# Optimization experiments

Hardware: AMD Instinct MI355X
Metric: run time of the kernel (lower is better)

Reference implementation:

```python
import jax, jax.numpy as jnp
import numpy as np

HIDDEN = 512
HEADS = 8
HEAD_DIM = HIDDEN // HEADS


def setup_inputs() -> dict:
    key = jax.random.key(0)
    ks = jax.random.split(key, 9)
    B, S = 4, 2048
    scale = 1.0 / np.sqrt(HIDDEN)
    x = jax.random.normal(ks[0], (B, S, HIDDEN), dtype=jnp.float32)
    Wq = jax.random.normal(ks[1], (HIDDEN, HIDDEN), dtype=jnp.float32) * scale
    Wk = jax.random.normal(ks[2], (HIDDEN, HIDDEN), dtype=jnp.float32) * scale
    Wv = jax.random.normal(ks[3], (HIDDEN, HIDDEN), dtype=jnp.float32) * scale
    Wo = jax.random.normal(ks[4], (HIDDEN, HIDDEN), dtype=jnp.float32) * scale
    bq = jax.random.normal(ks[5], (HIDDEN,), dtype=jnp.float32) * 0.01
    bk = jax.random.normal(ks[6], (HIDDEN,), dtype=jnp.float32) * 0.01
    bv = jax.random.normal(ks[7], (HIDDEN,), dtype=jnp.float32) * 0.01
    bo = jax.random.normal(ks[8], (HIDDEN,), dtype=jnp.float32) * 0.01
    return {"x": x, "Wq": Wq, "bq": bq, "Wk": Wk, "bk": bk,
            "Wv": Wv, "bv": bv, "Wo": Wo, "bo": bo}


def reference(x, Wq, bq, Wk, bk, Wv, bv, Wo, bo):
    B, S, _ = x.shape
    # project and split heads: [B, H, S, D]
    def split_heads(t):
        return t.reshape(B, S, HEADS, HEAD_DIM).transpose(0, 2, 1, 3)
    Q = split_heads(x @ Wq.T + bq)
    K = split_heads(x @ Wk.T + bk)
    V = split_heads(x @ Wv.T + bv)
    scores = jnp.einsum("bhsd,bhtd->bhst", Q, K) / jnp.sqrt(
        jnp.array(HEAD_DIM, dtype=x.dtype))
    attn = jax.nn.softmax(scores, axis=-1)  # dropout is identity in eval
    ctx = jnp.einsum("bhst,bhtd->bhsd", attn, V)
    ctx = ctx.transpose(0, 2, 1, 3).reshape(B, S, HIDDEN)
    return ctx @ Wo.T + bo
```

## Files before the change

kernel.cpp:

```cpp
#include <hip/hip_runtime.h>
#include <stdint.h>

#define HID 512
#define NH 8
#define HD 64
#define BB 4
#define SS 2048

typedef unsigned short u16;
typedef __attribute__((ext_vector_type(8))) short short8;
typedef __attribute__((ext_vector_type(4))) float f32x4;

#define MFMA16(a, b, c) __builtin_amdgcn_mfma_f32_16x16x32_bf16((a), (b), (c), 0, 0, 0)

__device__ __forceinline__ u16 f2bf(float f) {
  union { float f; uint32_t u; } v; v.f = f;
  return (u16)((v.u + 0x7fffu + ((v.u >> 16) & 1u)) >> 16);
}

__device__ __forceinline__ void gl_lds16(const u16* g, u16* l) {
  __builtin_amdgcn_global_load_lds(
      (const __attribute__((address_space(1))) unsigned int*)g,
      (__attribute__((address_space(3))) unsigned int*)l, 16, 0, 0);
}

__global__ void prep(const float* __restrict__ x,
                     const float* __restrict__ w0, const float* __restrict__ w1,
                     const float* __restrict__ w2, const float* __restrict__ w3,
                     u16* __restrict__ xb,
                     u16* __restrict__ o0, u16* __restrict__ o1,
                     u16* __restrict__ o2, u16* __restrict__ o3) {
  const int bid = blockIdx.x;
  const float* in;
  u16* out;
  int base;
  if (bid < 4096) {
    in = x; out = xb; base = bid * 1024;
  } else {
    const int z = (bid - 4096) >> 8;
    base = ((bid - 4096) & 255) * 1024;
    in = (z == 0) ? w0 : (z == 1) ? w1 : (z == 2) ? w2 : w3;
    out = (z == 0) ? o0 : (z == 1) ? o1 : (z == 2) ? o2 : o3;
  }
  const int i = base + threadIdx.x * 4;
  float4 v = *(const float4*)(in + i);
  ushort4 o;
  o.x = f2bf(v.x); o.y = f2bf(v.y); o.z = f2bf(v.z); o.w = f2bf(v.w);
  *(ushort4*)(out + i) = o;
}

__global__ __launch_bounds__(256, 3)
void qkv_gemm(const u16* __restrict__ xb,
              const u16* __restrict__ wq, const u16* __restrict__ wk, const u16* __restrict__ wv,
              const float* __restrict__ bq, const float* __restrict__ bk, const float* __restrict__ bv,
              u16* __restrict__ Q, u16* __restrict__ K, u16* __restrict__ Vt) {
  __shared__ u16 sA[2][128 * 32];
  __shared__ u16 sB[2][128 * 32];
  const int tid = threadIdx.x;
  const int lane = tid & 63;
  const int wave = tid >> 6;
  const int l15 = lane & 15;
  const int quad = lane >> 4;
  const int wm = wave >> 1, wn = wave & 1;
  const int z = blockIdx.z;

  const float* bias = (z == 0) ? bq : (z == 1) ? bk : bv;
  const float scale = (z == 0) ? 0.18033688011112042f : 1.0f;

  const u16* Arows = (z == 2) ? wv : xb;
  const u16* Brows = (z == 2) ? xb : ((z == 0) ? wq : wk);
  const int am0 = (z == 2) ? (blockIdx.y * 128) : (blockIdx.x * 128);
  const int bn0 = (z == 2) ? (blockIdx.x * 128) : (blockIdx.y * 128);

  const int srow = tid >> 2;
  const int sg = (tid & 3) ^ ((srow >> 1) & 3);
  const u16* gA = Arows + (am0 + srow) * 512 + sg * 8;
  const u16* gB = Brows + (bn0 + srow) * 512 + sg * 8;

  const int fsw = (quad ^ ((l15 >> 1) & 3)) * 8;
  int aoff[4], boff[4];
#pragma unroll
  for (int t = 0; t < 4; ++t) {
    aoff[t] = (wm * 64 + t * 16 + l15) * 32 + fsw;
    boff[t] = (wn * 64 + t * 16 + l15) * 32 + fsw;
  }

  f32x4 acc[4][4] = {};

  gl_lds16(gA, &sA[0][wave * 512]);
  gl_lds16(gA + 64 * 512, &sA[0][2048 + wave * 512]);
  gl_lds16(gB, &sB[0][wave * 512]);
  gl_lds16(gB + 64 * 512, &sB[0][2048 + wave * 512]);
  __syncthreads();

  for (int kk = 0; kk < 16; ++kk) {
    const int cur = kk & 1;
    if (kk < 15) {
      const int nxt = cur ^ 1;
      const int k0 = (kk + 1) * 32;
      gl_lds16(gA + k0, &sA[nxt][wave * 512]);
      gl_lds16(gA + k0 + 64 * 512, &sA[nxt][2048 + wave * 512]);
      gl_lds16(gB + k0, &sB[nxt][wave * 512]);
      gl_lds16(gB + k0 + 64 * 512, &sB[nxt][2048 + wave * 512]);
    }
    short8 af[4], bf[4];
#pragma unroll
    for (int t = 0; t < 4; ++t) af[t] = *(const short8*)&sA[cur][aoff[t]];
#pragma unroll
    for (int t = 0; t < 4; ++t) bf[t] = *(const short8*)&sB[cur][boff[t]];
#pragma unroll
    for (int mi = 0; mi < 4; ++mi)
#pragma unroll
      for (int ni = 0; ni < 4; ++ni)
        acc[mi][ni] = MFMA16(af[mi], bf[ni], acc[mi][ni]);
    __syncthreads();
  }

  if (z != 2) {
    u16* dst = (z == 0) ? Q : K;
#pragma unroll
    for (int mi = 0; mi < 4; ++mi) {
#pragma unroll
      for (int ni = 0; ni < 4; ++ni) {
        const int col = bn0 + wn * 64 + ni * 16 + l15;
        const float bs = bias[col];
#pragma unroll
        for (int i = 0; i < 4; ++i) {
          const int row = am0 + wm * 64 + mi * 16 + quad * 4 + i;
          const float v = (acc[mi][ni][i] + bs) * scale;
          const int b = row >> 11, s = row & 2047;
          const int h = col >> 6, d = col & 63;
          dst[(((size_t)(b * 8 + h) * 2048 + s) << 6) + d] = f2bf(v);
        }
      }
    }
  } else {
#pragma unroll
    for (int mi = 0; mi < 4; ++mi) {
#pragma unroll
      for (int i = 0; i < 4; ++i) {
        const int o = am0 + wm * 64 + mi * 16 + quad * 4 + i;
        const float bs = bias[o];
        const int h = o >> 6, d = o & 63;
#pragma unroll
        for (int ni = 0; ni < 4; ++ni) {
          const int r = bn0 + wn * 64 + ni * 16 + l15;
          const int b = r >> 11, s = r & 2047;
          Vt[(((size_t)(b * 8 + h) * 64 + d) << 11) + s] = f2bf(acc[mi][ni][i] + bs);
        }
      }
    }
  }
}

__global__ __launch_bounds__(512, 4)
void attn(const u16* __restrict__ Q, const u16* __restrict__ K,
          const u16* __restrict__ Vt, u16* __restrict__ ctx) {
  __shared__ u16 sK[2][64 * 64];
  __shared__ u16 sV[2][64 * 64];
  __shared__ u16 sP[128 * 64];
  const int tid = threadIdx.x;
  const int lane = tid & 63;
  const int wave = tid >> 6;
  const int l15 = lane & 15;
  const int quad = lane >> 4;
  const int qt = blockIdx.x;
  const int bh = blockIdx.y;

  const u16* Qb = Q + (size_t)bh * SS * HD;
  const u16* Kb = K + (size_t)bh * SS * HD;
  const u16* Vb = Vt + (size_t)bh * HD * SS;

  short8 qf[2];
  {
    const int r = qt * 128 + wave * 16 + l15;
    qf[0] = *(const short8*)(Qb + r * 64 + quad * 8);
    qf[1] = *(const short8*)(Qb + r * 64 + 32 + quad * 8);
  }

  short8 ones;
#pragma unroll
  for (int j = 0; j < 8; ++j) ones[j] = (short)0x3F80;

  f32x4 oacc[4] = {};
  f32x4 lsum = {};

  const int prow = (wave * 16 + l15) * 64;
  int xp[2];
#pragma unroll
  for (int kt = 0; kt < 2; ++kt) xp[kt] = ((kt * 4 + quad) ^ (l15 & 7)) * 8;

  const int tK = tid >> 3;
  const int dcK = (tid & 7) ^ (tK & 7);
  const u16* gK = Kb + tK * 64 + dcK * 8;
  const u16* gV = Vb + tK * 2048 + dcK * 8;

  gl_lds16(gK, &sK[0][wave * 512]);
  gl_lds16(gV, &sV[0][wave * 512]);
  __syncthreads();

  for (int tt = 0; tt < 32; ++tt) {
    const int cur = tt & 1;
    if (tt < 31) {
      const int nxt = cur ^ 1;
      gl_lds16(gK + (tt + 1) * 4096, &sK[nxt][wave * 512]);
      gl_lds16(gV + (tt + 1) * 64, &sV[nxt][wave * 512]);
    }

    f32x4 sacc[4] = {};
#pragma unroll
    for (int ni = 0; ni < 4; ++ni) {
      const short8 b0 = *(const short8*)&sK[cur][(ni * 16 + l15) * 64 + ((quad) ^ (l15 & 7)) * 8];
      const short8 b1 = *(const short8*)&sK[cur][(ni * 16 + l15) * 64 + ((4 + quad) ^ (l15 & 7)) * 8];
      sacc[ni] = MFMA16(qf[0], b0, sacc[ni]);
      sacc[ni] = MFMA16(qf[1], b1, sacc[ni]);
    }

#pragma unroll
    for (int i = 0; i < 4; ++i) {
      const int wrow = wave * 16 + quad * 4 + i;
      const int rx7 = (quad * 4 + i) & 7;
      const int base = wrow * 64 + (l15 & 7);
#pragma unroll
      for (int ni = 0; ni < 4; ++ni) {
        const float p = __builtin_amdgcn_exp2f(sacc[ni][i]);
        const uint32_t u = __builtin_bit_cast(uint32_t, p);
        sP[base + (((ni * 2 + (l15 >> 3)) ^ rx7) << 3)] = (u16)(u >> 16);
      }
    }

#pragma unroll
    for (int kt = 0; kt < 2; ++kt) {
      const short8 a = *(const short8*)&sP[prow + xp[kt]];
      lsum = MFMA16(a, ones, lsum);
#pragma unroll
      for (int nd = 0; nd < 4; ++nd) {
        const short8 bvv = *(const short8*)&sV[cur][(nd * 16 + l15) * 64 +
                                                   ((kt * 4 + quad) ^ (l15 & 7)) * 8];
        oacc[nd] = MFMA16(a, bvv, oacc[nd]);
      }
    }
    __syncthreads();
  }

  float inv[4];
#pragma unroll
  for (int i = 0; i < 4; ++i) inv[i] = __builtin_amdgcn_rcpf(lsum[i]);

  const int b = bh >> 3, h = bh & 7;
#pragma unroll
  for (int nd = 0; nd < 4; ++nd)
#pragma unroll
    for (int i = 0; i < 4; ++i) {
      const int s = qt * 128 + wave * 16 + quad * 4 + i;
      const int d = nd * 16 + l15;
      const float v = oacc[nd][i] * inv[i];
      ctx[((size_t)(b * 2048 + s) << 9) + h * 64 + d] = f2bf(v);
    }
}

__global__ __launch_bounds__(256, 2)
void out_gemm(const u16* __restrict__ A, const u16* __restrict__ W,
              const float* __restrict__ bias, float* __restrict__ out) {
  __shared__ u16 sA[2][128 * 32];
  __shared__ u16 sB[2][64 * 32];
  const int tid = threadIdx.x;
  const int lane = tid & 63;
  const int wave = tid >> 6;
  const int l15 = lane & 15;
  const int quad = lane >> 4;
  const int bm = blockIdx.x, bn = blockIdx.y;

  const int srow = tid >> 2;
  const int sg = (tid & 3) ^ ((srow >> 1) & 3);
  const u16* gA = A + (bm * 128 + srow) * 512 + sg * 8;
  const u16* gB = W + (bn * 64 + srow) * 512 + sg * 8;

  const int fsw = (quad ^ ((l15 >> 1) & 3)) * 8;
  int aoff[2], boff[4];
#pragma unroll
  for (int t = 0; t < 2; ++t) aoff[t] = (wave * 32 + t * 16 + l15) * 32 + fsw;
#pragma unroll
  for (int t = 0; t < 4; ++t) boff[t] = (t * 16 + l15) * 32 + fsw;

  f32x4 acc[2][4] = {};

  gl_lds16(gA, &sA[0][wave * 512]);
  gl_lds16(gA + 64 * 512, &sA[0][2048 + wave * 512]);
  gl_lds16(gB, &sB[0][wave * 512]);
  __syncthreads();

  for (int kk = 0; kk < 16; ++kk) {
    const int cur = kk & 1;
    if (kk < 15) {
      const int nxt = cur ^ 1;
      const int k0 = (kk + 1) * 32;
      gl_lds16(gA + k0, &sA[nxt][wave * 512]);
      gl_lds16(gA + k0 + 64 * 512, &sA[nxt][2048 + wave * 512]);
      gl_lds16(gB + k0, &sB[nxt][wave * 512]);
    }
    short8 af[2], bf[4];
#pragma unroll
    for (int t = 0; t < 2; ++t) af[t] = *(const short8*)&sA[cur][aoff[t]];
#pragma unroll
    for (int t = 0; t < 4; ++t) bf[t] = *(const short8*)&sB[cur][boff[t]];
#pragma unroll
    for (int mi = 0; mi < 2; ++mi)
#pragma unroll
      for (int ni = 0; ni < 4; ++ni)
        acc[mi][ni] = MFMA16(af[mi], bf[ni], acc[mi][ni]);
    __syncthreads();
  }

#pragma unroll
  for (int mi = 0; mi < 2; ++mi) {
#pragma unroll
    for (int ni = 0; ni < 4; ++ni) {
      const int col = bn * 64 + ni * 16 + l15;
      const float bs = bias[col];
#pragma unroll
      for (int i = 0; i < 4; ++i) {
        const int row = bm * 128 + wave * 32 + mi * 16 + quad * 4 + i;
        out[(size_t)row * 512 + col] = acc[mi][ni][i] + bs;
      }
    }
  }
}

extern "C" void kernel_launch(void* const* d_in, const int* in_sizes, int n_in,
                              void* d_out, int out_size, void* d_ws, size_t ws_size,
                              hipStream_t stream) {
  const float* x = (const float*)d_in[0];
  const float* Wq = (const float*)d_in[1];
  const float* bq = (const float*)d_in[2];
  const float* Wk = (const float*)d_in[3];
  const float* bk = (const float*)d_in[4];
  const float* Wv = (const float*)d_in[5];
  const float* bv = (const float*)d_in[6];
  const float* Wo = (const float*)d_in[7];
  const float* bo = (const float*)d_in[8];
  float* out = (float*)d_out;

  char* ws = (char*)d_ws;
  u16* xb  = (u16*)(ws);
  u16* wqb = (u16*)(ws + (8u << 20));
  u16* wkb = (u16*)(ws + (8u << 20) + (512u << 10));
  u16* wvb = (u16*)(ws + (9u << 20));
  u16* wob = (u16*)(ws + (9u << 20) + (512u << 10));
  u16* Qb  = (u16*)(ws + (10u << 20));
  u16* Kb  = (u16*)(ws + (18u << 20));
  u16* Vtb = (u16*)(ws + (26u << 20));
  u16* ctx = (u16*)(ws + (34u << 20));

  prep<<<5120, 256, 0, stream>>>(x, Wq, Wk, Wv, Wo, xb, wqb, wkb, wvb, wob);
  qkv_gemm<<<dim3(64, 4, 3), 256, 0, stream>>>(xb, wqb, wkb, wvb, bq, bk, bv, Qb, Kb, Vtb);
  attn<<<dim3(16, 32), 512, 0, stream>>>(Qb, Kb, Vtb, ctx);
  out_gemm<<<dim3(64, 8), 256, 0, stream>>>(ctx, wob, bo, out);
}
```

Before: 169.6 us.

## Deepen LDS pipelines with vmcnt waits and remap blocks to XCDs

Replaces the double-buffered LDS loads in the QKV GEMM, attention and output GEMM with triple/quad buffering. Each loop now waits on a partial vmcnt and a single barrier instead of a full __syncthreads, so more global->LDS loads stay in flight. It also flattens the grids and remaps block IDs so blocks that share data land on the same XCD, to improve L2 reuse. Costs are more LDS per block, which may lower occupancy, and correctness now depends on hand-written waitcnt encodings and barrier placement.

```diff
diff --git a/kernel.cpp b/kernel.cpp
--- a/kernel.cpp
+++ b/kernel.cpp
@@ -12,6 +12,11 @@
 typedef __attribute__((ext_vector_type(4))) float f32x4;
 
 #define MFMA16(a, b, c) __builtin_amdgcn_mfma_f32_16x16x32_bf16((a), (b), (c), 0, 0, 0)
+
+#define WAIT_VM4() __builtin_amdgcn_s_waitcnt(0xF74)
+#define WAIT_VM3() __builtin_amdgcn_s_waitcnt(0xF73)
+#define PIPE_BARRIER() do { asm volatile("" ::: "memory"); \
+  __builtin_amdgcn_s_barrier(); asm volatile("" ::: "memory"); } while (0)
 
 __device__ __forceinline__ u16 f2bf(float f) {
   union { float f; uint32_t u; } v; v.f = f;
@@ -54,23 +59,30 @@
               const u16* __restrict__ wq, const u16* __restrict__ wk, const u16* __restrict__ wv,
               const float* __restrict__ bq, const float* __restrict__ bk, const float* __restrict__ bv,
               u16* __restrict__ Q, u16* __restrict__ K, u16* __restrict__ Vt) {
-  __shared__ u16 sA[2][128 * 32];
-  __shared__ u16 sB[2][128 * 32];
+  __shared__ u16 sA[3][4096];
+  __shared__ u16 sB[3][4096];
   const int tid = threadIdx.x;
   const int lane = tid & 63;
   const int wave = tid >> 6;
   const int l15 = lane & 15;
   const int quad = lane >> 4;
   const int wm = wave >> 1, wn = wave & 1;
-  const int z = blockIdx.z;
+
+  const int L = blockIdx.x;
+  const int xcd = L & 7;
+  const int slot = L >> 3;
+  const int bm = xcd * 8 + (slot & 7);
+  const int r2 = slot >> 3;
+  const int bn = r2 & 3;
+  const int z = r2 >> 2;
 
   const float* bias = (z == 0) ? bq : (z == 1) ? bk : bv;
   const float scale = (z == 0) ? 0.18033688011112042f : 1.0f;
 
   const u16* Arows = (z == 2) ? wv : xb;
   const u16* Brows = (z == 2) ? xb : ((z == 0) ? wq : wk);
-  const int am0 = (z == 2) ? (blockIdx.y * 128) : (blockIdx.x * 128);
-  const int bn0 = (z == 2) ? (blockIdx.x * 128) : (blockIdx.y * 128);
+  const int am0 = (z == 2) ? (bn * 128) : (bm * 128);
+  const int bn0 = (z == 2) ? (bm * 128) : (bn * 128);
 
   const int srow = tid >> 2;
   const int sg = (tid & 3) ^ ((srow >> 1) & 3);
@@ -87,22 +99,28 @@
 
   f32x4 acc[4][4] = {};
 
-  gl_lds16(gA, &sA[0][wave * 512]);
-  gl_lds16(gA + 64 * 512, &sA[0][2048 + wave * 512]);
-  gl_lds16(gB, &sB[0][wave * 512]);
-  gl_lds16(gB + 64 * 512, &sB[0][2048 + wave * 512]);
-  __syncthreads();
+#pragma unroll
+  for (int t = 0; t < 2; ++t) {
+    const int k0 = t * 32;
+    gl_lds16(gA + k0, &sA[t][wave * 512]);
+    gl_lds16(gA + k0 + 64 * 512, &sA[t][2048 + wave * 512]);
+    gl_lds16(gB + k0, &sB[t][wave * 512]);
+    gl_lds16(gB + k0 + 64 * 512, &sB[t][2048 + wave * 512]);
+  }
 
   for (int kk = 0; kk < 16; ++kk) {
-    const int cur = kk & 1;
-    if (kk < 15) {
-      const int nxt = cur ^ 1;
-      const int k0 = (kk + 1) * 32;
-      gl_lds16(gA + k0, &sA[nxt][wave * 512]);
-      gl_lds16(gA + k0 + 64 * 512, &sA[nxt][2048 + wave * 512]);
-      gl_lds16(gB + k0, &sB[nxt][wave * 512]);
-      gl_lds16(gB + k0 + 64 * 512, &sB[nxt][2048 + wave * 512]);
-    }
+    WAIT_VM4();
+    PIPE_BARRIER();
+    {
+      const int tp = (kk + 2 < 16) ? kk + 2 : 15;
+      const int ns = (kk + 2) % 3;
+      const int k0 = tp * 32;
+      gl_lds16(gA + k0, &sA[ns][wave * 512]);
+      gl_lds16(gA + k0 + 64 * 512, &sA[ns][2048 + wave * 512]);
+      gl_lds16(gB + k0, &sB[ns][wave * 512]);
+      gl_lds16(gB + k0 + 64 * 512, &sB[ns][2048 + wave * 512]);
+    }
+    const int cur = kk % 3;
     short8 af[4], bf[4];
 #pragma unroll
     for (int t = 0; t < 4; ++t) af[t] = *(const short8*)&sA[cur][aoff[t]];
@@ -113,7 +131,6 @@
 #pragma unroll
       for (int ni = 0; ni < 4; ++ni)
         acc[mi][ni] = MFMA16(af[mi], bf[ni], acc[mi][ni]);
-    __syncthreads();
   }
 
   if (z != 2) {
@@ -156,16 +173,20 @@
 __global__ __launch_bounds__(512, 4)
 void attn(const u16* __restrict__ Q, const u16* __restrict__ K,
           const u16* __restrict__ Vt, u16* __restrict__ ctx) {
-  __shared__ u16 sK[2][64 * 64];
-  __shared__ u16 sV[2][64 * 64];
-  __shared__ u16 sP[128 * 64];
+  __shared__ u16 sK[4][4096];
+  __shared__ u16 sV[4][4096];
+  __shared__ u16 sP[8192];
   const int tid = threadIdx.x;
   const int lane = tid & 63;
   const int wave = tid >> 6;
   const int l15 = lane & 15;
   const int quad = lane >> 4;
-  const int qt = blockIdx.x;
-  const int bh = blockIdx.y;
+
+  const int L = blockIdx.x;
+  const int xcd = L & 7;
+  const int slot = L >> 3;
+  const int bh = xcd * 4 + (slot & 3);
+  const int qt = slot >> 2;
 
   const u16* Qb = Q + (size_t)bh * SS * HD;
   const u16* Kb = K + (size_t)bh * SS * HD;
@@ -177,6 +198,7 @@
     qf[0] = *(const short8*)(Qb + r * 64 + quad * 8);
     qf[1] = *(const short8*)(Qb + r * 64 + 32 + quad * 8);
   }
+  asm volatile("" ::: "memory");
 
   short8 ones;
 #pragma unroll
@@ -195,17 +217,22 @@
   const u16* gK = Kb + tK * 64 + dcK * 8;
   const u16* gV = Vb + tK * 2048 + dcK * 8;
 
-  gl_lds16(gK, &sK[0][wave * 512]);
-  gl_lds16(gV, &sV[0][wave * 512]);
-  __syncthreads();
+#pragma unroll
+  for (int t = 0; t < 3; ++t) {
+    gl_lds16(gK + t * 4096, &sK[t][wave * 512]);
+    gl_lds16(gV + t * 64, &sV[t][wave * 512]);
+  }
 
   for (int tt = 0; tt < 32; ++tt) {
-    const int cur = tt & 1;
-    if (tt < 31) {
-      const int nxt = cur ^ 1;
-      gl_lds16(gK + (tt + 1) * 4096, &sK[nxt][wave * 512]);
-      gl_lds16(gV + (tt + 1) * 64, &sV[nxt][wave * 512]);
-    }
+    WAIT_VM4();
+    PIPE_BARRIER();
+    {
+      const int tp = (tt + 3 < 32) ? tt + 3 : 31;
+      const int ns = (tt + 3) & 3;
+      gl_lds16(gK + tp * 4096, &sK[ns][wave * 512]);
+      gl_lds16(gV + tp * 64, &sV[ns][wave * 512]);
+    }
+    const int cur = tt & 3;
 
     f32x4 sacc[4] = {};
 #pragma unroll
@@ -240,7 +267,6 @@
         oacc[nd] = MFMA16(a, bvv, oacc[nd]);
       }
     }
-    __syncthreads();
   }
 
   float inv[4];
@@ -262,14 +288,19 @@
 __global__ __launch_bounds__(256, 2)
 void out_gemm(const u16* __restrict__ A, const u16* __restrict__ W,
               const float* __restrict__ bias, float* __restrict__ out) {
-  __shared__ u16 sA[2][128 * 32];
-  __shared__ u16 sB[2][64 * 32];
+  __shared__ u16 sA[3][4096];
+  __shared__ u16 sB[3][2048];
   const int tid = threadIdx.x;
   const int lane = tid & 63;
   const int wave = tid >> 6;
   const int l15 = lane & 15;
   const int quad = lane >> 4;
-  const int bm = blockIdx.x, bn = blockIdx.y;
+
+  const int L = blockIdx.x;
+  const int xcd = L & 7;
+  const int slot = L >> 3;
+  const int bm = xcd * 8 + (slot & 7);
+  const int bn = slot >> 3;
 
   const int srow = tid >> 2;
   const int sg = (tid & 3) ^ ((srow >> 1) & 3);
@@ -285,20 +316,26 @@
 
   f32x4 acc[2][4] = {};
 
-  gl_lds16(gA, &sA[0][wave * 512]);
-  gl_lds16(gA + 64 * 512, &sA[0][2048 + wave * 512]);
-  gl_lds16(gB, &sB[0][wave * 512]);
-  __syncthreads();
+#pragma unroll
+  for (int t = 0; t < 2; ++t) {
+    const int k0 = t * 32;
+    gl_lds16(gA + k0, &sA[t][wave * 512]);
+    gl_lds16(gA + k0 + 64 * 512, &sA[t][2048 + wave * 512]);
+    gl_lds16(gB + k0, &sB[t][wave * 512]);
+  }
 
   for (int kk = 0; kk < 16; ++kk) {
-    const int cur = kk & 1;
-    if (kk < 15) {
-      const int nxt = cur ^ 1;
-      const int k0 = (kk + 1) * 32;
-      gl_lds16(gA + k0, &sA[nxt][wave * 512]);
-      gl_lds16(gA + k0 + 64 * 512, &sA[nxt][2048 + wave * 512]);
-      gl_lds16(gB + k0, &sB[nxt][wave * 512]);
-    }
+    WAIT_VM3();
+    PIPE_BARRIER();
+    {
+      const int tp = (kk + 2 < 16) ? kk + 2 : 15;
+      const int ns = (kk + 2) % 3;
+      const int k0 = tp * 32;
+      gl_lds16(gA + k0, &sA[ns][wave * 512]);
+      gl_lds16(gA + k0 + 64 * 512, &sA[ns][2048 + wave * 512]);
+      gl_lds16(gB + k0, &sB[ns][wave * 512]);
+    }
+    const int cur = kk % 3;
     short8 af[2], bf[4];
 #pragma unroll
     for (int t = 0; t < 2; ++t) af[t] = *(const short8*)&sA[cur][aoff[t]];
@@ -309,7 +346,6 @@
 #pragma unroll
       for (int ni = 0; ni < 4; ++ni)
         acc[mi][ni] = MFMA16(af[mi], bf[ni], acc[mi][ni]);
-    __syncthreads();
   }
 
 #pragma unroll
@@ -353,7 +389,7 @@
   u16* ctx = (u16*)(ws + (34u << 20));
 
   prep<<<5120, 256, 0, stream>>>(x, Wq, Wk, Wv, Wo, xb, wqb, wkb, wvb, wob);
-  qkv_gemm<<<dim3(64, 4, 3), 256, 0, stream>>>(xb, wqb, wkb, wvb, bq, bk, bv, Qb, Kb, Vtb);
-  attn<<<dim3(16, 32), 512, 0, stream>>>(Qb, Kb, Vtb, ctx);
-  out_gemm<<<dim3(64, 8), 256, 0, stream>>>(ctx, wob, bo, out);
-}
+  qkv_gemm<<<768, 256, 0, stream>>>(xb, wqb, wkb, wvb, bq, bk, bv, Qb, Kb, Vtb);
+  attn<<<512, 512, 0, stream>>>(Qb, Kb, Vtb, ctx);
+  out_gemm<<<512, 256, 0, stream>>>(ctx, wob, bo, out);
+}
```

Measured after the change: 164.9 us. -2.8%, faster.
